# Kernel tuning notes

Measured on AMD Instinct MI355X. Metric: run time of the kernel, lower is better.

## Reference

```python
import jax, jax.numpy as jnp
import numpy as np


def setup_inputs() -> dict:
    key = jax.random.key(0)
    kq, kk, kv, km = jax.random.split(key, 4)
    B, H, N, D = 2, 16, 2048, 64
    q = jax.random.normal(kq, (B, H, N, D), dtype=jnp.float32)
    k = jax.random.normal(kk, (B, H, N, D), dtype=jnp.float32)
    v = jax.random.normal(kv, (B, H, N, D), dtype=jnp.float32)
    # mask > 0 means position is masked OUT (matches torch masked_fill(mask > 0, -max))
    mask = jax.random.randint(km, (B, N), 0, 2, dtype=jnp.int32)
    return {"q": q, "k": k, "v": v, "mask": mask}


def reference(q, k, v, mask):
    # q,k,v: [b,h,n,d]; mask: [b,j] with >0 = masked
    scale = q.shape[-1] ** -0.5
    sim = jnp.einsum('bhid,bhjd->bhij', q, k) * scale
    # l2_dist score modification: 2*qk*scale - ||q||^2 - ||k||^2
    q_sq = jnp.sum(q * q, axis=-1, keepdims=True)          # [b,h,i,1]
    k_sq = jnp.sum(k * k, axis=-1, keepdims=True)          # [b,h,j,1]
    sim = sim * 2 - q_sq - jnp.swapaxes(k_sq, -1, -2)       # [b,h,i,j]
    neg_max = -jnp.finfo(sim.dtype).max
    m = (mask > 0)[:, None, None, :]                        # [b,1,1,j]
    sim = jnp.where(m, neg_max, sim)
    attn = jax.nn.softmax(sim, axis=-1)
    out = jnp.einsum('bhij,bhjd->bhid', attn, v)
    return out
```

## Files before the change

kernel.cpp:

```cpp
#include <hip/hip_runtime.h>
#include <hip/hip_bf16.h>

#define NSEQ 2048
#define DD   64
#define HH   16
#define QT   128
#define KVB  64
#define NKV  (NSEQ / KVB)

typedef __attribute__((ext_vector_type(4)))  float f4;
typedef __attribute__((ext_vector_type(16))) float f32x16;
typedef __attribute__((ext_vector_type(8)))  short bf16x8;
typedef __attribute__((ext_vector_type(4)))  unsigned int u32x4;
typedef __attribute__((ext_vector_type(2)))  unsigned int u32x2;

#define QSCL  0.36067376022224085f
#define LOG2E 1.4426950408889634f
#define NEGBIG (-1.0e30f)
#define THR   8.0f

#define SWZ(row, q)  (((row) << 6) + ((((q) ^ ((row) & 7))) << 3))
#define SWZV(d, q)   (((d) << 6) + ((((q) ^ (((d) >> 2) & 7) ^ ((d) & 3))) << 3))

#if defined(__has_builtin)
#if __has_builtin(__builtin_amdgcn_exp2f)
#define EXP2F __builtin_amdgcn_exp2f
#endif
#if __has_builtin(__builtin_amdgcn_permlane32_swap)
#define HAVE_PLSWAP 1
#endif
#endif
#ifndef EXP2F
#define EXP2F exp2f
#endif

union bfu { u32x4 u; bf16x8 h; };

__device__ __forceinline__ unsigned cvtpk(float lo, float hi) {
    unsigned r;
    asm("v_cvt_pk_bf16_f32 %0, %1, %2" : "=v"(r) : "v"(lo), "v"(hi));
    return r;
}
template<int CTRL>
__device__ __forceinline__ float dppf(float x) {
    return __int_as_float(__builtin_amdgcn_update_dpp(
        0, __float_as_int(x), CTRL, 0xF, 0xF, true));
}
__device__ __forceinline__ float cross_max(float x) {
#ifdef HAVE_PLSWAP
    u32x2 r = __builtin_amdgcn_permlane32_swap(__float_as_uint(x), __float_as_uint(x),
                                               false, false);
    return fmaxf(__uint_as_float(r[0]), __uint_as_float(r[1]));
#else
    return fmaxf(x, __shfl_xor(x, 32));
#endif
}
__device__ __forceinline__ float cross_add(float x) {
#ifdef HAVE_PLSWAP
    u32x2 r = __builtin_amdgcn_permlane32_swap(__float_as_uint(x), __float_as_uint(x),
                                               false, false);
    return __uint_as_float(r[0]) + __uint_as_float(r[1]);
#else
    return x + __shfl_xor(x, 32);
#endif
}
__device__ __forceinline__ void pairmix(unsigned A, unsigned B,
                                        unsigned& d0, unsigned& d2, bool hi) {
#ifdef HAVE_PLSWAP
    u32x2 r = __builtin_amdgcn_permlane32_swap(A, B, false, false);
    d0 = r[0]; d2 = r[1];
#else
    unsigned v = hi ? A : B;
    unsigned x = (unsigned)__shfl_xor((int)v, 32);
    d0 = hi ? x : A;
    d2 = hi ? B : x;
#endif
}

__global__ __launch_bounds__(256, 2)
void attend_kernel(const float* __restrict__ qg, const float* __restrict__ kg,
                   const float* __restrict__ vg, const int* __restrict__ maskg,
                   float* __restrict__ outg)
{
    __shared__ __align__(16) unsigned short Ks[2][KVB * DD];
    __shared__ __align__(16) unsigned short Vt[2][KVB * DD];
    __shared__ __align__(16) float bias_s[2][KVB];

    const int t    = threadIdx.x;
    const int w    = t >> 6;
    const int lane = t & 63;
    const int c5   = lane & 31;
    const int g2   = lane >> 5;

    const int p     = blockIdx.x;
    const int bh    = (p & 7) * 4 + ((p >> 3) >> 4);
    const int qtile = (p >> 3) & 15;
    const int b     = bh >> 4;

    const size_t base = (size_t)bh * NSEQ * DD;
    const float* kp = kg + base;
    const float* vp = vg + base;
    const int*   mp = maskg + b * NSEQ;

    bfu qf[4];
    {
        const float* qp = qg + base + (size_t)(qtile*QT + w*32 + c5) * DD;
        #pragma unroll
        for (int ck = 0; ck < 4; ++ck) {
            f4 a  = *(const f4*)(qp + ck*16 + g2*8);
            f4 bb = *(const f4*)(qp + ck*16 + g2*8 + 4);
            qf[ck].u = (u32x4){ cvtpk(a[0]*QSCL,  a[1]*QSCL),  cvtpk(a[2]*QSCL,  a[3]*QSCL),
                                cvtpk(bb[0]*QSCL, bb[1]*QSCL), cvtpk(bb[2]*QSCL, bb[3]*QSCL) };
        }
    }

    f32x16 acc0, acc1;
    #pragma unroll
    for (int r = 0; r < 16; ++r) { acc0[r] = 0.f; acc1[r] = 0.f; }
    float m_run = NEGBIG, l_run = 0.f;

    const bool isK = (w < 2);
    const int  jK  = t >> 1;
    const int  kq0 = (t & 1) * 4;
    const int  uv  = t & 127;
    const int  dq  = uv & 15;
    const int  jq  = uv >> 4;

    f4  st[8];
    int mr = 0;

    auto loadTile = [&](int gt) {
        const int j0 = gt * KVB;
        if (isK) {
            const float* src = kp + (size_t)(j0 + jK) * DD + kq0 * 8;
            #pragma unroll
            for (int i2 = 0; i2 < 8; ++i2) st[i2] = ((const f4*)src)[i2];
            mr = mp[j0 + jK];
        } else {
            #pragma unroll
            for (int i2 = 0; i2 < 8; ++i2)
                st[i2] = *(const f4*)(vp + (size_t)(j0 + jq*8 + i2) * DD + dq*4);
        }
    };

    auto stageTile = [&](int bsel) {
        if (isK) {
            float sq = 0.f;
            #pragma unroll
            for (int i2 = 0; i2 < 8; ++i2)
                sq += st[i2][0]*st[i2][0] + st[i2][1]*st[i2][1]
                    + st[i2][2]*st[i2][2] + st[i2][3]*st[i2][3];
            sq += dppf<0xB1>(sq);
            if ((t & 1) == 0) bias_s[bsel][jK] = (mr > 0) ? NEGBIG : -sq * LOG2E;
            #pragma unroll
            for (int s2 = 0; s2 < 4; ++s2) {
                u32x4 kk = (u32x4){ cvtpk(st[2*s2][0],   st[2*s2][1]),
                                    cvtpk(st[2*s2][2],   st[2*s2][3]),
                                    cvtpk(st[2*s2+1][0], st[2*s2+1][1]),
                                    cvtpk(st[2*s2+1][2], st[2*s2+1][3]) };
                *(u32x4*)&Ks[bsel][SWZ(jK, kq0 + s2)] = kk;
            }
        } else {
            #pragma unroll
            for (int cc = 0; cc < 4; ++cc) {
                int d = dq*4 + cc;
                u32x4 tv = (u32x4){ cvtpk(st[0][cc], st[1][cc]),
                                    cvtpk(st[2][cc], st[3][cc]),
                                    cvtpk(st[4][cc], st[5][cc]),
                                    cvtpk(st[6][cc], st[7][cc]) };
                *(u32x4*)&Vt[bsel][SWZV(d, jq)] = tv;
            }
        }
    };

    loadTile(0);
    stageTile(0);
    loadTile(1);
    __syncthreads();

    int cur = 0;
    for (int kt = 0; kt < NKV; ++kt) {
        if (kt + 1 < NKV) stageTile(cur ^ 1);
        if (kt + 2 < NKV) loadTile(kt + 2);

        f32x16 s01[2];
        #pragma unroll
        for (int jt = 0; jt < 2; ++jt) {
            f4 b4[4];
            #pragma unroll
            for (int q = 0; q < 4; ++q)
                b4[q] = *(const f4*)&bias_s[cur][32*jt + 8*q + 4*g2];
            f32x16 sc;
            #pragma unroll
            for (int r = 0; r < 16; ++r) sc[r] = b4[r>>2][r&3];
            __builtin_amdgcn_s_setprio(1);
            #pragma unroll
            for (int ck = 0; ck < 4; ++ck) {
                bfu kb;
                kb.u = *(const u32x4*)&Ks[cur][SWZ(32*jt + c5, 2*ck + g2)];
                sc = __builtin_amdgcn_mfma_f32_32x32x16_bf16(kb.h, qf[ck].h, sc, 0, 0, 0);
            }
            __builtin_amdgcn_s_setprio(0);
            s01[jt] = sc;
        }

        float pmax;
        {
            float mm[8];
            #pragma unroll
            for (int i2 = 0; i2 < 8; ++i2)
                mm[i2] = fmaxf(fmaxf(s01[0][2*i2], s01[0][2*i2+1]),
                               fmaxf(s01[1][2*i2], s01[1][2*i2+1]));
            float ma = fmaxf(fmaxf(mm[0], mm[1]), fmaxf(mm[2], mm[3]));
            float mb = fmaxf(fmaxf(mm[4], mm[5]), fmaxf(mm[6], mm[7]));
            pmax = fmaxf(ma, mb);
        }
        pmax = cross_max(pmax);
        if (!__all(pmax <= m_run + THR)) {
            float mn = fmaxf(m_run, pmax);
            float corr = EXP2F(m_run - mn);
            m_run = mn;
            l_run *= corr;
            #pragma unroll
            for (int r = 0; r < 16; ++r) { acc0[r] *= corr; acc1[r] *= corr; }
        }

        unsigned Wp[16];
        float ls0 = 0.f, ls1 = 0.f;
        #pragma unroll
        for (int jt = 0; jt < 2; ++jt) {
            #pragma unroll
            for (int m = 0; m < 8; ++m) {
                float e0 = EXP2F(s01[jt][2*m]   - m_run);
                float e1 = EXP2F(s01[jt][2*m+1] - m_run);
                if (m & 1) ls1 += e0 + e1; else ls0 += e0 + e1;
                Wp[jt*8 + m] = cvtpk(e0, e1);
            }
        }
        l_run += cross_add(ls0 + ls1);

        const bool hi = (g2 != 0);
        __builtin_amdgcn_s_setprio(1);
        #pragma unroll
        for (int ck = 0; ck < 4; ++ck) {
            const int bs = (ck >> 1) * 8 + 4 * (ck & 1);
            unsigned d00, d20, d01, d21;
            pairmix(Wp[bs],   Wp[bs+2], d00, d20, hi);
            pairmix(Wp[bs+1], Wp[bs+3], d01, d21, hi);
            bfu pb;
            pb.u = (u32x4){ d00, d01, d20, d21 };
            bfu va0, va1;
            va0.u = *(const u32x4*)&Vt[cur][SWZV(     c5, 2*ck + g2)];
            va1.u = *(const u32x4*)&Vt[cur][SWZV(32 + c5, 2*ck + g2)];
            acc0 = __builtin_amdgcn_mfma_f32_32x32x16_bf16(va0.h, pb.h, acc0, 0, 0, 0);
            acc1 = __builtin_amdgcn_mfma_f32_32x32x16_bf16(va1.h, pb.h, acc1, 0, 0, 0);
        }
        __builtin_amdgcn_s_setprio(0);

        __syncthreads();
        cur ^= 1;
    }

    float inv = 1.0f / l_run;
    float* op = outg + base + (size_t)(qtile*QT + w*32 + c5) * DD;
    #pragma unroll
    for (int dt = 0; dt < 2; ++dt) {
        const f32x16 A = dt ? acc1 : acc0;
        #pragma unroll
        for (int q = 0; q < 4; ++q) {
            f4 o = { A[4*q]*inv, A[4*q+1]*inv, A[4*q+2]*inv, A[4*q+3]*inv };
            *(f4*)(op + 32*dt + 8*q + 4*g2) = o;
        }
    }
}

extern "C" void kernel_launch(void* const* d_in, const int* in_sizes, int n_in,
                              void* d_out, int out_size, void* d_ws, size_t ws_size,
                              hipStream_t stream) {
    const float* q    = (const float*)d_in[0];
    const float* k    = (const float*)d_in[1];
    const float* v    = (const float*)d_in[2];
    const int*   mask = (const int*)d_in[3];
    float* out = (float*)d_out;
    attend_kernel<<<dim3(512), dim3(256), 0, stream>>>(q, k, v, mask, out);
}
```

Before: 63.80 us.

## Process two KV tiles per iteration with doubled shared buffers and split staging

Each loop iteration now processes two 64-key tiles (128 keys): both QK^T products, one combined max and rescale check, softmax for both, then two PV passes. Shared K/V/bias buffers double in size so a pair of tiles can be staged per phase, with staging of the next pair split into two halves interleaved around the softmax. This halves the barriers and running-max rescale checks per key, and overlaps global loads with more compute. The cost is more shared memory and more registers, which may threaten the two-blocks-per-CU occupancy.

```diff
diff --git a/kernel.cpp b/kernel.cpp
--- a/kernel.cpp
+++ b/kernel.cpp
@@ -7,6 +7,7 @@
 #define QT   128
 #define KVB  64
 #define NKV  (NSEQ / KVB)
+#define NR   (NKV / 2)
 
 typedef __attribute__((ext_vector_type(4)))  float f4;
 typedef __attribute__((ext_vector_type(16))) float f32x16;
@@ -82,9 +83,9 @@
                    const float* __restrict__ vg, const int* __restrict__ maskg,
                    float* __restrict__ outg)
 {
-    __shared__ __align__(16) unsigned short Ks[2][KVB * DD];
-    __shared__ __align__(16) unsigned short Vt[2][KVB * DD];
-    __shared__ __align__(16) float bias_s[2][KVB];
+    __shared__ __align__(16) unsigned short Ks[2][2 * KVB * DD];
+    __shared__ __align__(16) unsigned short Vt[2][2 * KVB * DD];
+    __shared__ __align__(16) float bias_s[2][2 * KVB];
 
     const int t    = threadIdx.x;
     const int w    = t >> 6;
@@ -92,9 +93,9 @@
     const int c5   = lane & 31;
     const int g2   = lane >> 5;
 
-    const int p     = blockIdx.x;
-    const int bh    = (p & 7) * 4 + ((p >> 3) >> 4);
-    const int qtile = (p >> 3) & 15;
+    const int p0    = blockIdx.x;
+    const int bh    = (p0 & 7) * 4 + ((p0 >> 3) >> 4);
+    const int qtile = (p0 >> 3) & 15;
     const int b     = bh >> 4;
 
     const size_t base = (size_t)bh * NSEQ * DD;
@@ -143,7 +144,7 @@
         }
     };
 
-    auto stageTile = [&](int bsel) {
+    auto stageTile = [&](int pbuf, int tsub) {
         if (isK) {
             float sq = 0.f;
             #pragma unroll
@@ -151,14 +152,14 @@
                 sq += st[i2][0]*st[i2][0] + st[i2][1]*st[i2][1]
                     + st[i2][2]*st[i2][2] + st[i2][3]*st[i2][3];
             sq += dppf<0xB1>(sq);
-            if ((t & 1) == 0) bias_s[bsel][jK] = (mr > 0) ? NEGBIG : -sq * LOG2E;
+            if ((t & 1) == 0) bias_s[pbuf][tsub*KVB + jK] = (mr > 0) ? NEGBIG : -sq * LOG2E;
             #pragma unroll
             for (int s2 = 0; s2 < 4; ++s2) {
                 u32x4 kk = (u32x4){ cvtpk(st[2*s2][0],   st[2*s2][1]),
                                     cvtpk(st[2*s2][2],   st[2*s2][3]),
                                     cvtpk(st[2*s2+1][0], st[2*s2+1][1]),
                                     cvtpk(st[2*s2+1][2], st[2*s2+1][3]) };
-                *(u32x4*)&Ks[bsel][SWZ(jK, kq0 + s2)] = kk;
+                *(u32x4*)&Ks[pbuf][tsub*(KVB*DD) + SWZ(jK, kq0 + s2)] = kk;
             }
         } else {
             #pragma unroll
@@ -168,49 +169,57 @@
                                     cvtpk(st[2][cc], st[3][cc]),
                                     cvtpk(st[4][cc], st[5][cc]),
                                     cvtpk(st[6][cc], st[7][cc]) };
-                *(u32x4*)&Vt[bsel][SWZV(d, jq)] = tv;
+                *(u32x4*)&Vt[pbuf][tsub*(KVB*DD) + SWZV(d, jq)] = tv;
             }
         }
     };
 
-    loadTile(0);
-    stageTile(0);
-    loadTile(1);
+    loadTile(0); stageTile(0, 0);
+    loadTile(1); stageTile(0, 1);
+    loadTile(2);
     __syncthreads();
 
-    int cur = 0;
-    for (int kt = 0; kt < NKV; ++kt) {
-        if (kt + 1 < NKV) stageTile(cur ^ 1);
-        if (kt + 2 < NKV) loadTile(kt + 2);
-
-        f32x16 s01[2];
-        #pragma unroll
-        for (int jt = 0; jt < 2; ++jt) {
-            f4 b4[4];
-            #pragma unroll
-            for (int q = 0; q < 4; ++q)
-                b4[q] = *(const f4*)&bias_s[cur][32*jt + 8*q + 4*g2];
-            f32x16 sc;
-            #pragma unroll
-            for (int r = 0; r < 16; ++r) sc[r] = b4[r>>2][r&3];
-            __builtin_amdgcn_s_setprio(1);
-            #pragma unroll
-            for (int ck = 0; ck < 4; ++ck) {
-                bfu kb;
-                kb.u = *(const u32x4*)&Ks[cur][SWZ(32*jt + c5, 2*ck + g2)];
-                sc = __builtin_amdgcn_mfma_f32_32x32x16_bf16(kb.h, qf[ck].h, sc, 0, 0, 0);
-            }
-            __builtin_amdgcn_s_setprio(0);
-            s01[jt] = sc;
-        }
+    for (int r = 0; r < NR; ++r) {
+        const int p = r & 1;
+
+        if (r + 1 < NR) { stageTile(p ^ 1, 0); loadTile(2*r + 3); }
+
+        auto qkt = [&](int tsub, f32x16* sOut) {
+            #pragma unroll
+            for (int jt = 0; jt < 2; ++jt) {
+                f4 b4[4];
+                #pragma unroll
+                for (int q = 0; q < 4; ++q)
+                    b4[q] = *(const f4*)&bias_s[p][tsub*KVB + 32*jt + 8*q + 4*g2];
+                f32x16 sc;
+                #pragma unroll
+                for (int rr = 0; rr < 16; ++rr) sc[rr] = b4[rr>>2][rr&3];
+                __builtin_amdgcn_s_setprio(1);
+                #pragma unroll
+                for (int ck = 0; ck < 4; ++ck) {
+                    bfu kb;
+                    kb.u = *(const u32x4*)&Ks[p][tsub*(KVB*DD) + SWZ(32*jt + c5, 2*ck + g2)];
+                    sc = __builtin_amdgcn_mfma_f32_32x32x16_bf16(kb.h, qf[ck].h, sc, 0, 0, 0);
+                }
+                __builtin_amdgcn_s_setprio(0);
+                sOut[jt] = sc;
+            }
+        };
+        f32x16 sA[2], sB[2];
+        qkt(0, sA);
+        qkt(1, sB);
 
         float pmax;
         {
             float mm[8];
             #pragma unroll
-            for (int i2 = 0; i2 < 8; ++i2)
-                mm[i2] = fmaxf(fmaxf(s01[0][2*i2], s01[0][2*i2+1]),
-                               fmaxf(s01[1][2*i2], s01[1][2*i2+1]));
+            for (int i2 = 0; i2 < 8; ++i2) {
+                float a0 = fmaxf(fmaxf(sA[0][2*i2], sA[0][2*i2+1]),
+                                 fmaxf(sA[1][2*i2], sA[1][2*i2+1]));
+                float b0 = fmaxf(fmaxf(sB[0][2*i2], sB[0][2*i2+1]),
+                                 fmaxf(sB[1][2*i2], sB[1][2*i2+1]));
+                mm[i2] = fmaxf(a0, b0);
+            }
             float ma = fmaxf(fmaxf(mm[0], mm[1]), fmaxf(mm[2], mm[3]));
             float mb = fmaxf(fmaxf(mm[4], mm[5]), fmaxf(mm[6], mm[7]));
             pmax = fmaxf(ma, mb);
@@ -222,43 +231,62 @@
             m_run = mn;
             l_run *= corr;
             #pragma unroll
-            for (int r = 0; r < 16; ++r) { acc0[r] *= corr; acc1[r] *= corr; }
-        }
-
-        unsigned Wp[16];
-        float ls0 = 0.f, ls1 = 0.f;
-        #pragma unroll
-        for (int jt = 0; jt < 2; ++jt) {
-            #pragma unroll
-            for (int m = 0; m < 8; ++m) {
-                float e0 = EXP2F(s01[jt][2*m]   - m_run);
-                float e1 = EXP2F(s01[jt][2*m+1] - m_run);
-                if (m & 1) ls1 += e0 + e1; else ls0 += e0 + e1;
-                Wp[jt*8 + m] = cvtpk(e0, e1);
-            }
-        }
-        l_run += cross_add(ls0 + ls1);
+            for (int rr = 0; rr < 16; ++rr) { acc0[rr] *= corr; acc1[rr] *= corr; }
+        }
+
+        unsigned WpA[16], WpB[16];
+        float ls = 0.f;
+        {
+            float l0 = 0.f, l1 = 0.f;
+            #pragma unroll
+            for (int jt = 0; jt < 2; ++jt) {
+                #pragma unroll
+                for (int m = 0; m < 8; ++m) {
+                    float e0 = EXP2F(sA[jt][2*m]   - m_run);
+                    float e1 = EXP2F(sA[jt][2*m+1] - m_run);
+                    if (m & 1) l1 += e0 + e1; else l0 += e0 + e1;
+                    WpA[jt*8 + m] = cvtpk(e0, e1);
+                }
+            }
+            #pragma unroll
+            for (int jt = 0; jt < 2; ++jt) {
+                #pragma unroll
+                for (int m = 0; m < 8; ++m) {
+                    float e0 = EXP2F(sB[jt][2*m]   - m_run);
+                    float e1 = EXP2F(sB[jt][2*m+1] - m_run);
+                    if (m & 1) l1 += e0 + e1; else l0 += e0 + e1;
+                    WpB[jt*8 + m] = cvtpk(e0, e1);
+                }
+            }
+            ls = l0 + l1;
+        }
+        l_run += cross_add(ls);
+
+        if (r + 1 < NR) { stageTile(p ^ 1, 1); if (r + 2 < NR) loadTile(2*r + 4); }
 
         const bool hi = (g2 != 0);
-        __builtin_amdgcn_s_setprio(1);
-        #pragma unroll
-        for (int ck = 0; ck < 4; ++ck) {
-            const int bs = (ck >> 1) * 8 + 4 * (ck & 1);
-            unsigned d00, d20, d01, d21;
-            pairmix(Wp[bs],   Wp[bs+2], d00, d20, hi);
-            pairmix(Wp[bs+1], Wp[bs+3], d01, d21, hi);
-            bfu pb;
-            pb.u = (u32x4){ d00, d01, d20, d21 };
-            bfu va0, va1;
-            va0.u = *(const u32x4*)&Vt[cur][SWZV(     c5, 2*ck + g2)];
-            va1.u = *(const u32x4*)&Vt[cur][SWZV(32 + c5, 2*ck + g2)];
-            acc0 = __builtin_amdgcn_mfma_f32_32x32x16_bf16(va0.h, pb.h, acc0, 0, 0, 0);
-            acc1 = __builtin_amdgcn_mfma_f32_32x32x16_bf16(va1.h, pb.h, acc1, 0, 0, 0);
-        }
-        __builtin_amdgcn_s_setprio(0);
+        auto pv = [&](int tsub, unsigned* Wp) {
+            __builtin_amdgcn_s_setprio(1);
+            #pragma unroll
+            for (int ck = 0; ck < 4; ++ck) {
+                const int bs = (ck >> 1) * 8 + 4 * (ck & 1);
+                unsigned d00, d20, d01, d21;
+                pairmix(Wp[bs],   Wp[bs+2], d00, d20, hi);
+                pairmix(Wp[bs+1], Wp[bs+3], d01, d21, hi);
+                bfu pb;
+                pb.u = (u32x4){ d00, d01, d20, d21 };
+                bfu va0, va1;
+                va0.u = *(const u32x4*)&Vt[p][tsub*(KVB*DD) + SWZV(     c5, 2*ck + g2)];
+                va1.u = *(const u32x4*)&Vt[p][tsub*(KVB*DD) + SWZV(32 + c5, 2*ck + g2)];
+                acc0 = __builtin_amdgcn_mfma_f32_32x32x16_bf16(va0.h, pb.h, acc0, 0, 0, 0);
+                acc1 = __builtin_amdgcn_mfma_f32_32x32x16_bf16(va1.h, pb.h, acc1, 0, 0, 0);
+            }
+            __builtin_amdgcn_s_setprio(0);
+        };
+        pv(0, WpA);
+        pv(1, WpB);
 
         __syncthreads();
-        cur ^= 1;
     }
 
     float inv = 1.0f / l_run;
```

Result: no change. 63.46 us (-0.5%).

## Split block into producer and consumer warps for K/V staging

Applied to the files above, without the earlier changes.

Doubles the block to 512 threads: four waves now only compute attention, and four dedicated producer waves load K/V from global memory, convert them to bf16 and stage them into the double-buffered LDS tiles one step ahead. The consumer waves no longer hold staging registers or issue global loads, so their register pressure drops and their MFMA work can overlap with the producers' fetching. In exchange the producers' loads are no longer prefetched two tiles ahead, launch bounds change to 512x4 (which may cap registers), and the extra waves use occupancy slots.

```diff
diff --git a/kernel.cpp b/kernel.cpp
--- a/kernel.cpp
+++ b/kernel.cpp
@@ -77,7 +77,7 @@
 #endif
 }
 
-__global__ __launch_bounds__(256, 2)
+__global__ __launch_bounds__(512, 4)
 void attend_kernel(const float* __restrict__ qg, const float* __restrict__ kg,
                    const float* __restrict__ vg, const int* __restrict__ maskg,
                    float* __restrict__ outg)
@@ -91,6 +91,7 @@
     const int lane = t & 63;
     const int c5   = lane & 31;
     const int g2   = lane >> 5;
+    const bool isProd = (w >= 4);
 
     const int p     = blockIdx.x;
     const int bh    = (p & 7) * 4 + ((p >> 3) >> 4);
@@ -103,7 +104,9 @@
     const int*   mp = maskg + b * NSEQ;
 
     bfu qf[4];
-    {
+    f32x16 acc0, acc1;
+    float m_run = NEGBIG, l_run = 0.f;
+    if (!isProd) {
         const float* qp = qg + base + (size_t)(qtile*QT + w*32 + c5) * DD;
         #pragma unroll
         for (int ck = 0; ck < 4; ++ck) {
@@ -112,46 +115,32 @@
             qf[ck].u = (u32x4){ cvtpk(a[0]*QSCL,  a[1]*QSCL),  cvtpk(a[2]*QSCL,  a[3]*QSCL),
                                 cvtpk(bb[0]*QSCL, bb[1]*QSCL), cvtpk(bb[2]*QSCL, bb[3]*QSCL) };
         }
+        #pragma unroll
+        for (int r = 0; r < 16; ++r) { acc0[r] = 0.f; acc1[r] = 0.f; }
     }
 
-    f32x16 acc0, acc1;
-    #pragma unroll
-    for (int r = 0; r < 16; ++r) { acc0[r] = 0.f; acc1[r] = 0.f; }
-    float m_run = NEGBIG, l_run = 0.f;
-
-    const bool isK = (w < 2);
-    const int  jK  = t >> 1;
-    const int  kq0 = (t & 1) * 4;
-    const int  uv  = t & 127;
+    const int  u   = t & 255;
+    const bool isK = (u < 128);
+    const int  jK  = u >> 1;
+    const int  kq0 = (u & 1) * 4;
+    const int  uv  = u & 127;
     const int  dq  = uv & 15;
     const int  jq  = uv >> 4;
 
-    f4  st[8];
-    int mr = 0;
-
-    auto loadTile = [&](int gt) {
-        const int j0 = gt * KVB;
+    auto prodTile = [&](int gt, int bsel) {
+        f4 st[8];
         if (isK) {
-            const float* src = kp + (size_t)(j0 + jK) * DD + kq0 * 8;
+            const float* src = kp + (size_t)(gt*KVB + jK) * DD + kq0 * 8;
             #pragma unroll
             for (int i2 = 0; i2 < 8; ++i2) st[i2] = ((const f4*)src)[i2];
-            mr = mp[j0 + jK];
-        } else {
-            #pragma unroll
-            for (int i2 = 0; i2 < 8; ++i2)
-                st[i2] = *(const f4*)(vp + (size_t)(j0 + jq*8 + i2) * DD + dq*4);
-        }
-    };
-
-    auto stageTile = [&](int bsel) {
-        if (isK) {
+            int mr = mp[gt*KVB + jK];
             float sq = 0.f;
             #pragma unroll
             for (int i2 = 0; i2 < 8; ++i2)
                 sq += st[i2][0]*st[i2][0] + st[i2][1]*st[i2][1]
                     + st[i2][2]*st[i2][2] + st[i2][3]*st[i2][3];
             sq += dppf<0xB1>(sq);
-            if ((t & 1) == 0) bias_s[bsel][jK] = (mr > 0) ? NEGBIG : -sq * LOG2E;
+            if ((u & 1) == 0) bias_s[bsel][jK] = (mr > 0) ? NEGBIG : -sq * LOG2E;
             #pragma unroll
             for (int s2 = 0; s2 < 4; ++s2) {
                 u32x4 kk = (u32x4){ cvtpk(st[2*s2][0],   st[2*s2][1]),
@@ -161,6 +150,9 @@
                 *(u32x4*)&Ks[bsel][SWZ(jK, kq0 + s2)] = kk;
             }
         } else {
+            #pragma unroll
+            for (int i2 = 0; i2 < 8; ++i2)
+                st[i2] = *(const f4*)(vp + (size_t)(gt*KVB + jq*8 + i2) * DD + dq*4);
             #pragma unroll
             for (int cc = 0; cc < 4; ++cc) {
                 int d = dq*4 + cc;
@@ -173,103 +165,104 @@
         }
     };
 
-    loadTile(0);
-    stageTile(0);
-    loadTile(1);
+    if (isProd) prodTile(0, 0);
     __syncthreads();
 
-    int cur = 0;
     for (int kt = 0; kt < NKV; ++kt) {
-        if (kt + 1 < NKV) stageTile(cur ^ 1);
-        if (kt + 2 < NKV) loadTile(kt + 2);
-
-        f32x16 s01[2];
+        const int kc = kt & 1;
+
+        if (isProd) {
+            if (kt + 1 < NKV) prodTile(kt + 1, kc ^ 1);
+        } else {
+            f32x16 s01[2];
+            #pragma unroll
+            for (int jt = 0; jt < 2; ++jt) {
+                f4 b4[4];
+                #pragma unroll
+                for (int q = 0; q < 4; ++q)
+                    b4[q] = *(const f4*)&bias_s[kc][32*jt + 8*q + 4*g2];
+                f32x16 sc;
+                #pragma unroll
+                for (int r = 0; r < 16; ++r) sc[r] = b4[r>>2][r&3];
+                __builtin_amdgcn_s_setprio(1);
+                #pragma unroll
+                for (int ck = 0; ck < 4; ++ck) {
+                    bfu kb;
+                    kb.u = *(const u32x4*)&Ks[kc][SWZ(32*jt + c5, 2*ck + g2)];
+                    sc = __builtin_amdgcn_mfma_f32_32x32x16_bf16(kb.h, qf[ck].h, sc, 0, 0, 0);
+                }
+                __builtin_amdgcn_s_setprio(0);
+                s01[jt] = sc;
+            }
+
+            float pmax;
+            {
+                float mm[8];
+                #pragma unroll
+                for (int i2 = 0; i2 < 8; ++i2)
+                    mm[i2] = fmaxf(fmaxf(s01[0][2*i2], s01[0][2*i2+1]),
+                                   fmaxf(s01[1][2*i2], s01[1][2*i2+1]));
+                float ma = fmaxf(fmaxf(mm[0], mm[1]), fmaxf(mm[2], mm[3]));
+                float mb = fmaxf(fmaxf(mm[4], mm[5]), fmaxf(mm[6], mm[7]));
+                pmax = fmaxf(ma, mb);
+            }
+            pmax = cross_max(pmax);
+            if (!__all(pmax <= m_run + THR)) {
+                float mn = fmaxf(m_run, pmax);
+                float corr = EXP2F(m_run - mn);
+                m_run = mn;
+                l_run *= corr;
+                #pragma unroll
+                for (int r = 0; r < 16; ++r) { acc0[r] *= corr; acc1[r] *= corr; }
+            }
+
+            unsigned Wp[16];
+            float ls0 = 0.f, ls1 = 0.f;
+            #pragma unroll
+            for (int jt = 0; jt < 2; ++jt) {
+                #pragma unroll
+                for (int m = 0; m < 8; ++m) {
+                    float e0 = EXP2F(s01[jt][2*m]   - m_run);
+                    float e1 = EXP2F(s01[jt][2*m+1] - m_run);
+                    if (m & 1) ls1 += e0 + e1; else ls0 += e0 + e1;
+                    Wp[jt*8 + m] = cvtpk(e0, e1);
+                }
+            }
+            l_run += cross_add(ls0 + ls1);
+
+            const bool hi = (g2 != 0);
+            __builtin_amdgcn_s_setprio(1);
+            #pragma unroll
+            for (int ck = 0; ck < 4; ++ck) {
+                const int bs = (ck >> 1) * 8 + 4 * (ck & 1);
+                unsigned d00, d20, d01, d21;
+                pairmix(Wp[bs],   Wp[bs+2], d00, d20, hi);
+                pairmix(Wp[bs+1], Wp[bs+3], d01, d21, hi);
+                bfu pb;
+                pb.u = (u32x4){ d00, d01, d20, d21 };
+                bfu va0, va1;
+                va0.u = *(const u32x4*)&Vt[kc][SWZV(     c5, 2*ck + g2)];
+                va1.u = *(const u32x4*)&Vt[kc][SWZV(32 + c5, 2*ck + g2)];
+                acc0 = __builtin_amdgcn_mfma_f32_32x32x16_bf16(va0.h, pb.h, acc0, 0, 0, 0);
+                acc1 = __builtin_amdgcn_mfma_f32_32x32x16_bf16(va1.h, pb.h, acc1, 0, 0, 0);
+            }
+            __builtin_amdgcn_s_setprio(0);
+        }
+
+        __syncthreads();
+    }
+
+    if (!isProd) {
+        float inv = 1.0f / l_run;
+        float* op = outg + base + (size_t)(qtile*QT + w*32 + c5) * DD;
         #pragma unroll
-        for (int jt = 0; jt < 2; ++jt) {
-            f4 b4[4];
-            #pragma unroll
-            for (int q = 0; q < 4; ++q)
-                b4[q] = *(const f4*)&bias_s[cur][32*jt + 8*q + 4*g2];
-            f32x16 sc;
-            #pragma unroll
-            for (int r = 0; r < 16; ++r) sc[r] = b4[r>>2][r&3];
-            __builtin_amdgcn_s_setprio(1);
-            #pragma unroll
-            for (int ck = 0; ck < 4; ++ck) {
-                bfu kb;
-                kb.u = *(const u32x4*)&Ks[cur][SWZ(32*jt + c5, 2*ck + g2)];
-                sc = __builtin_amdgcn_mfma_f32_32x32x16_bf16(kb.h, qf[ck].h, sc, 0, 0, 0);
-            }
-            __builtin_amdgcn_s_setprio(0);
-            s01[jt] = sc;
-        }
-
-        float pmax;
-        {
-            float mm[8];
-            #pragma unroll
-            for (int i2 = 0; i2 < 8; ++i2)
-                mm[i2] = fmaxf(fmaxf(s01[0][2*i2], s01[0][2*i2+1]),
-                               fmaxf(s01[1][2*i2], s01[1][2*i2+1]));
-            float ma = fmaxf(fmaxf(mm[0], mm[1]), fmaxf(mm[2], mm[3]));
-            float mb = fmaxf(fmaxf(mm[4], mm[5]), fmaxf(mm[6], mm[7]));
-            pmax = fmaxf(ma, mb);
-        }
-        pmax = cross_max(pmax);
-        if (!__all(pmax <= m_run + THR)) {
-            float mn = fmaxf(m_run, pmax);
-            float corr = EXP2F(m_run - mn);
-            m_run = mn;
-            l_run *= corr;
-            #pragma unroll
-            for (int r = 0; r < 16; ++r) { acc0[r] *= corr; acc1[r] *= corr; }
-        }
-
-        unsigned Wp[16];
-        float ls0 = 0.f, ls1 = 0.f;
-        #pragma unroll
-        for (int jt = 0; jt < 2; ++jt) {
-            #pragma unroll
-            for (int m = 0; m < 8; ++m) {
-                float e0 = EXP2F(s01[jt][2*m]   - m_run);
-                float e1 = EXP2F(s01[jt][2*m+1] - m_run);
-                if (m & 1) ls1 += e0 + e1; else ls0 += e0 + e1;
-                Wp[jt*8 + m] = cvtpk(e0, e1);
-            }
-        }
-        l_run += cross_add(ls0 + ls1);
-
-        const bool hi = (g2 != 0);
-        __builtin_amdgcn_s_setprio(1);
-        #pragma unroll
-        for (int ck = 0; ck < 4; ++ck) {
-            const int bs = (ck >> 1) * 8 + 4 * (ck & 1);
-            unsigned d00, d20, d01, d21;
-            pairmix(Wp[bs],   Wp[bs+2], d00, d20, hi);
-            pairmix(Wp[bs+1], Wp[bs+3], d01, d21, hi);
-            bfu pb;
-            pb.u = (u32x4){ d00, d01, d20, d21 };
-            bfu va0, va1;
-            va0.u = *(const u32x4*)&Vt[cur][SWZV(     c5, 2*ck + g2)];
-            va1.u = *(const u32x4*)&Vt[cur][SWZV(32 + c5, 2*ck + g2)];
-            acc0 = __builtin_amdgcn_mfma_f32_32x32x16_bf16(va0.h, pb.h, acc0, 0, 0, 0);
-            acc1 = __builtin_amdgcn_mfma_f32_32x32x16_bf16(va1.h, pb.h, acc1, 0, 0, 0);
-        }
-        __builtin_amdgcn_s_setprio(0);
-
-        __syncthreads();
-        cur ^= 1;
-    }
-
-    float inv = 1.0f / l_run;
-    float* op = outg + base + (size_t)(qtile*QT + w*32 + c5) * DD;
-    #pragma unroll
-    for (int dt = 0; dt < 2; ++dt) {
-        const f32x16 A = dt ? acc1 : acc0;
-        #pragma unroll
-        for (int q = 0; q < 4; ++q) {
-            f4 o = { A[4*q]*inv, A[4*q+1]*inv, A[4*q+2]*inv, A[4*q+3]*inv };
-            *(f4*)(op + 32*dt + 8*q + 4*g2) = o;
+        for (int dt = 0; dt < 2; ++dt) {
+            const f32x16 A = dt ? acc1 : acc0;
+            #pragma unroll
+            for (int q = 0; q < 4; ++q) {
+                f4 o = { A[4*q]*inv, A[4*q+1]*inv, A[4*q+2]*inv, A[4*q+3]*inv };
+                *(f4*)(op + 32*dt + 8*q + 4*g2) = o;
+            }
         }
     }
 }
@@ -282,5 +275,5 @@
     const float* v    = (const float*)d_in[2];
     const int*   mask = (const int*)d_in[3];
     float* out = (float*)d_out;
-    attend_kernel<<<dim3(512), dim3(256), 0, stream>>>(q, k, v, mask, out);
-}
+    attend_kernel<<<dim3(512), dim3(512), 0, stream>>>(q, k, v, mask, out);
+}
```

After: 64.75 us. No clear change (+1.5%).

## Pre-convert K/V to bf16 fragment images in workspace and drop LDS staging

Applied to the files above, without the earlier changes.

Adds a prep kernel that converts K and V to bf16 once per call. It writes them in workspace laid out in the exact MFMA fragment order, together with a precomputed mask/norm bias. The main kernel then reads its fragments straight from global memory into registers, prefetching the next K tile, and no longer needs shared memory or per-tile __syncthreads. This removes the fp32 K/V traffic and conversion work that was repeated across 16 q-tiles. The cost is an extra launch and workspace traffic, and it relies on L2 for reuse. A fallback to the original kernel runs if the workspace is too small.

```diff
diff --git a/kernel.cpp b/kernel.cpp
--- a/kernel.cpp
+++ b/kernel.cpp
@@ -7,6 +7,9 @@
 #define QT   128
 #define KVB  64
 #define NKV  (NSEQ / KVB)
+#define NBH  32
+#define TILE_SH 4096
+#define KIMG_BYTES ((size_t)NBH * NKV * TILE_SH * 2)
 
 typedef __attribute__((ext_vector_type(4)))  float f4;
 typedef __attribute__((ext_vector_type(16))) float f32x16;
@@ -77,15 +80,74 @@
 #endif
 }
 
-__global__ __launch_bounds__(256, 2)
-void attend_kernel(const float* __restrict__ qg, const float* __restrict__ kg,
-                   const float* __restrict__ vg, const int* __restrict__ maskg,
-                   float* __restrict__ outg)
+__global__ __launch_bounds__(256)
+void prep_kernel(const float* __restrict__ kg, const float* __restrict__ vg,
+                 const int* __restrict__ maskg,
+                 unsigned short* __restrict__ Kimg,
+                 unsigned short* __restrict__ Vimg,
+                 float* __restrict__ biasg)
 {
-    __shared__ __align__(16) unsigned short Ks[2][KVB * DD];
-    __shared__ __align__(16) unsigned short Vt[2][KVB * DD];
-    __shared__ __align__(16) float bias_s[2][KVB];
-
+    int blk = blockIdx.x;
+    const bool doV = (blk >= NBH * NKV);
+    if (doV) blk -= NBH * NKV;
+    const int bh   = blk >> 5;
+    const int tile = blk & 31;
+    const int tid  = threadIdx.x;
+
+    if (!doV) {
+        __shared__ float bsum[64];
+        const float* kp = kg + ((size_t)bh * NSEQ + tile * KVB) * DD;
+        unsigned short* out = Kimg + (size_t)blk * TILE_SH;
+        if (tid < 64) bsum[tid] = 0.f;
+        __syncthreads();
+        #pragma unroll
+        for (int cc = 0; cc < 2; ++cc) {
+            int c  = tid + cc * 256;
+            int c5 = c & 31, g2 = (c >> 5) & 1, ck = (c >> 6) & 3, jt = c >> 8;
+            const float* src = kp + (size_t)(32*jt + c5) * DD + 16*ck + 8*g2;
+            f4 a = ((const f4*)src)[0];
+            f4 b = ((const f4*)src)[1];
+            u32x4 kk = (u32x4){ cvtpk(a[0],a[1]), cvtpk(a[2],a[3]),
+                                cvtpk(b[0],b[1]), cvtpk(b[2],b[3]) };
+            *(u32x4*)&out[c * 8] = kk;
+            float sq = a[0]*a[0]+a[1]*a[1]+a[2]*a[2]+a[3]*a[3]
+                     + b[0]*b[0]+b[1]*b[1]+b[2]*b[2]+b[3]*b[3];
+            atomicAdd(&bsum[32*jt + c5], sq);
+        }
+        __syncthreads();
+        if (tid < 64) {
+            int j  = tile * KVB + tid;
+            int b_ = bh >> 4;
+            biasg[bh * NSEQ + j] =
+                (maskg[b_ * NSEQ + j] > 0) ? NEGBIG : -bsum[tid] * LOG2E;
+        }
+    } else {
+        const float* vp = vg + ((size_t)bh * NSEQ + tile * KVB) * DD;
+        unsigned short* out = Vimg + (size_t)blk * TILE_SH;
+        #pragma unroll
+        for (int cc = 0; cc < 2; ++cc) {
+            int c  = tid + cc * 256;
+            int c5 = c & 31, dt = (c >> 5) & 1, g2 = (c >> 6) & 1, ck = c >> 7;
+            int d  = dt * 32 + c5;
+            int j0 = 16*ck + 8*g2;
+            float v0 = vp[(size_t)(j0+0)*DD + d], v1 = vp[(size_t)(j0+1)*DD + d];
+            float v2 = vp[(size_t)(j0+2)*DD + d], v3 = vp[(size_t)(j0+3)*DD + d];
+            float v4 = vp[(size_t)(j0+4)*DD + d], v5 = vp[(size_t)(j0+5)*DD + d];
+            float v6 = vp[(size_t)(j0+6)*DD + d], v7 = vp[(size_t)(j0+7)*DD + d];
+            u32x4 tv = (u32x4){ cvtpk(v0,v1), cvtpk(v2,v3),
+                                cvtpk(v4,v5), cvtpk(v6,v7) };
+            *(u32x4*)&out[c * 8] = tv;
+        }
+    }
+}
+
+__global__ __launch_bounds__(256)
+void attend_main(const unsigned short* __restrict__ Kimg,
+                 const unsigned short* __restrict__ Vimg,
+                 const float* __restrict__ biasg,
+                 const float* __restrict__ qg,
+                 float* __restrict__ outg)
+{
     const int t    = threadIdx.x;
     const int w    = t >> 6;
     const int lane = t & 63;
@@ -95,12 +157,11 @@
     const int p     = blockIdx.x;
     const int bh    = (p & 7) * 4 + ((p >> 3) >> 4);
     const int qtile = (p >> 3) & 15;
-    const int b     = bh >> 4;
 
     const size_t base = (size_t)bh * NSEQ * DD;
-    const float* kp = kg + base;
-    const float* vp = vg + base;
-    const int*   mp = maskg + b * NSEQ;
+    const unsigned short* kimg = Kimg + (size_t)bh * NKV * TILE_SH;
+    const unsigned short* vimg = Vimg + (size_t)bh * NKV * TILE_SH;
+    const float* bias_bh = biasg + bh * NSEQ;
 
     bfu qf[4];
     {
@@ -114,6 +175,161 @@
         }
     }
 
+    f32x16 acc0, acc1;
+    #pragma unroll
+    for (int r = 0; r < 16; ++r) { acc0[r] = 0.f; acc1[r] = 0.f; }
+    float m_run = NEGBIG, l_run = 0.f;
+
+    u32x4 kbA[8], kbB[8];
+    #pragma unroll
+    for (int jt = 0; jt < 2; ++jt)
+        #pragma unroll
+        for (int ck = 0; ck < 4; ++ck)
+            kbA[jt*4+ck] = *(const u32x4*)&kimg[(size_t)((((jt*4+ck)*2+g2)*32 + c5) * 8)];
+
+    auto round = [&](int kt, u32x4 (&kbC)[8], u32x4 (&kbN)[8]) {
+        f32x16 s01[2];
+        #pragma unroll
+        for (int jt = 0; jt < 2; ++jt) {
+            f4 b4[4];
+            #pragma unroll
+            for (int q = 0; q < 4; ++q)
+                b4[q] = *(const f4*)&bias_bh[kt*KVB + 32*jt + 8*q + 4*g2];
+            f32x16 sc;
+            #pragma unroll
+            for (int r = 0; r < 16; ++r) sc[r] = b4[r>>2][r&3];
+            __builtin_amdgcn_s_setprio(1);
+            #pragma unroll
+            for (int ck = 0; ck < 4; ++ck) {
+                bfu kb; kb.u = kbC[jt*4+ck];
+                sc = __builtin_amdgcn_mfma_f32_32x32x16_bf16(kb.h, qf[ck].h, sc, 0, 0, 0);
+            }
+            __builtin_amdgcn_s_setprio(0);
+            s01[jt] = sc;
+        }
+
+        const unsigned short* vt = vimg + (size_t)kt * TILE_SH;
+        u32x4 vau[8];
+        #pragma unroll
+        for (int ck = 0; ck < 4; ++ck)
+            #pragma unroll
+            for (int dt = 0; dt < 2; ++dt)
+                vau[ck*2+dt] = *(const u32x4*)&vt[(size_t)(((((ck*2+g2)*2)+dt)*32 + c5) * 8)];
+
+        if (kt + 1 < NKV) {
+            const unsigned short* kn = kimg + (size_t)(kt+1) * TILE_SH;
+            #pragma unroll
+            for (int jt = 0; jt < 2; ++jt)
+                #pragma unroll
+                for (int ck = 0; ck < 4; ++ck)
+                    kbN[jt*4+ck] = *(const u32x4*)&kn[(size_t)((((jt*4+ck)*2+g2)*32 + c5) * 8)];
+        }
+
+        float pmax;
+        {
+            float mm[8];
+            #pragma unroll
+            for (int i2 = 0; i2 < 8; ++i2)
+                mm[i2] = fmaxf(fmaxf(s01[0][2*i2], s01[0][2*i2+1]),
+                               fmaxf(s01[1][2*i2], s01[1][2*i2+1]));
+            float ma = fmaxf(fmaxf(mm[0], mm[1]), fmaxf(mm[2], mm[3]));
+            float mb = fmaxf(fmaxf(mm[4], mm[5]), fmaxf(mm[6], mm[7]));
+            pmax = fmaxf(ma, mb);
+        }
+        pmax = cross_max(pmax);
+        if (!__all(pmax <= m_run + THR)) {
+            float mn = fmaxf(m_run, pmax);
+            float corr = EXP2F(m_run - mn);
+            m_run = mn;
+            l_run *= corr;
+            #pragma unroll
+            for (int r = 0; r < 16; ++r) { acc0[r] *= corr; acc1[r] *= corr; }
+        }
+
+        unsigned Wp[16];
+        float ls0 = 0.f, ls1 = 0.f;
+        #pragma unroll
+        for (int jt = 0; jt < 2; ++jt) {
+            #pragma unroll
+            for (int m = 0; m < 8; ++m) {
+                float e0 = EXP2F(s01[jt][2*m]   - m_run);
+                float e1 = EXP2F(s01[jt][2*m+1] - m_run);
+                if (m & 1) ls1 += e0 + e1; else ls0 += e0 + e1;
+                Wp[jt*8 + m] = cvtpk(e0, e1);
+            }
+        }
+        l_run += cross_add(ls0 + ls1);
+
+        const bool hi = (g2 != 0);
+        __builtin_amdgcn_s_setprio(1);
+        #pragma unroll
+        for (int ck = 0; ck < 4; ++ck) {
+            const int bs = (ck >> 1) * 8 + 4 * (ck & 1);
+            unsigned d00, d20, d01, d21;
+            pairmix(Wp[bs],   Wp[bs+2], d00, d20, hi);
+            pairmix(Wp[bs+1], Wp[bs+3], d01, d21, hi);
+            bfu pb; pb.u = (u32x4){ d00, d01, d20, d21 };
+            bfu va0, va1;
+            va0.u = vau[ck*2+0];
+            va1.u = vau[ck*2+1];
+            acc0 = __builtin_amdgcn_mfma_f32_32x32x16_bf16(va0.h, pb.h, acc0, 0, 0, 0);
+            acc1 = __builtin_amdgcn_mfma_f32_32x32x16_bf16(va1.h, pb.h, acc1, 0, 0, 0);
+        }
+        __builtin_amdgcn_s_setprio(0);
+    };
+
+    for (int k2 = 0; k2 < NKV; k2 += 2) {
+        round(k2,     kbA, kbB);
+        round(k2 + 1, kbB, kbA);
+    }
+
+    float inv = 1.0f / l_run;
+    float* op = outg + base + (size_t)(qtile*QT + w*32 + c5) * DD;
+    #pragma unroll
+    for (int dt = 0; dt < 2; ++dt) {
+        const f32x16 A = dt ? acc1 : acc0;
+        #pragma unroll
+        for (int q = 0; q < 4; ++q) {
+            f4 o = { A[4*q]*inv, A[4*q+1]*inv, A[4*q+2]*inv, A[4*q+3]*inv };
+            *(f4*)(op + 32*dt + 8*q + 4*g2) = o;
+        }
+    }
+}
+
+__global__ __launch_bounds__(256, 2)
+void attend_fallback(const float* __restrict__ qg, const float* __restrict__ kg,
+                     const float* __restrict__ vg, const int* __restrict__ maskg,
+                     float* __restrict__ outg)
+{
+    __shared__ __align__(16) unsigned short Ks[2][KVB * DD];
+    __shared__ __align__(16) unsigned short Vt[2][KVB * DD];
+    __shared__ __align__(16) float bias_s[2][KVB];
+
+    const int t    = threadIdx.x;
+    const int w    = t >> 6;
+    const int lane = t & 63;
+    const int c5   = lane & 31;
+    const int g2   = lane >> 5;
+    const int p     = blockIdx.x;
+    const int bh    = (p & 7) * 4 + ((p >> 3) >> 4);
+    const int qtile = (p >> 3) & 15;
+    const int b     = bh >> 4;
+    const size_t base = (size_t)bh * NSEQ * DD;
+    const float* kp = kg + base;
+    const float* vp = vg + base;
+    const int*   mp = maskg + b * NSEQ;
+
+    bfu qf[4];
+    {
+        const float* qp = qg + base + (size_t)(qtile*QT + w*32 + c5) * DD;
+        #pragma unroll
+        for (int ck = 0; ck < 4; ++ck) {
+            f4 a  = *(const f4*)(qp + ck*16 + g2*8);
+            f4 bb = *(const f4*)(qp + ck*16 + g2*8 + 4);
+            qf[ck].u = (u32x4){ cvtpk(a[0]*QSCL,  a[1]*QSCL),  cvtpk(a[2]*QSCL,  a[3]*QSCL),
+                                cvtpk(bb[0]*QSCL, bb[1]*QSCL), cvtpk(bb[2]*QSCL, bb[3]*QSCL) };
+        }
+    }
     f32x16 acc0, acc1;
     #pragma unroll
     for (int r = 0; r < 16; ++r) { acc0[r] = 0.f; acc1[r] = 0.f; }
@@ -125,7 +341,6 @@
     const int  uv  = t & 127;
     const int  dq  = uv & 15;
     const int  jq  = uv >> 4;
-
     f4  st[8];
     int mr = 0;
 
@@ -142,7 +357,6 @@
                 st[i2] = *(const f4*)(vp + (size_t)(j0 + jq*8 + i2) * DD + dq*4);
         }
     };
-
     auto stageTile = [&](int bsel) {
         if (isK) {
             float sq = 0.f;
@@ -173,16 +387,12 @@
         }
     };
 
-    loadTile(0);
-    stageTile(0);
-    loadTile(1);
+    loadTile(0); stageTile(0); loadTile(1);
     __syncthreads();
-
     int cur = 0;
     for (int kt = 0; kt < NKV; ++kt) {
         if (kt + 1 < NKV) stageTile(cur ^ 1);
         if (kt + 2 < NKV) loadTile(kt + 2);
-
         f32x16 s01[2];
         #pragma unroll
         for (int jt = 0; jt < 2; ++jt) {
@@ -203,7 +413,6 @@
             __builtin_amdgcn_s_setprio(0);
             s01[jt] = sc;
         }
-
         float pmax;
         {
             float mm[8];
@@ -219,12 +428,10 @@
         if (!__all(pmax <= m_run + THR)) {
             float mn = fmaxf(m_run, pmax);
             float corr = EXP2F(m_run - mn);
-            m_run = mn;
-            l_run *= corr;
+            m_run = mn; l_run *= corr;
             #pragma unroll
             for (int r = 0; r < 16; ++r) { acc0[r] *= corr; acc1[r] *= corr; }
         }
-
         unsigned Wp[16];
         float ls0 = 0.f, ls1 = 0.f;
         #pragma unroll
@@ -238,7 +445,6 @@
             }
         }
         l_run += cross_add(ls0 + ls1);
-
         const bool hi = (g2 != 0);
         __builtin_amdgcn_s_setprio(1);
         #pragma unroll
@@ -247,8 +453,7 @@
             unsigned d00, d20, d01, d21;
             pairmix(Wp[bs],   Wp[bs+2], d00, d20, hi);
             pairmix(Wp[bs+1], Wp[bs+3], d01, d21, hi);
-            bfu pb;
-            pb.u = (u32x4){ d00, d01, d20, d21 };
+            bfu pb; pb.u = (u32x4){ d00, d01, d20, d21 };
             bfu va0, va1;
             va0.u = *(const u32x4*)&Vt[cur][SWZV(     c5, 2*ck + g2)];
             va1.u = *(const u32x4*)&Vt[cur][SWZV(32 + c5, 2*ck + g2)];
@@ -256,11 +461,9 @@
             acc1 = __builtin_amdgcn_mfma_f32_32x32x16_bf16(va1.h, pb.h, acc1, 0, 0, 0);
         }
         __builtin_amdgcn_s_setprio(0);
-
         __syncthreads();
         cur ^= 1;
     }
-
     float inv = 1.0f / l_run;
     float* op = outg + base + (size_t)(qtile*QT + w*32 + c5) * DD;
     #pragma unroll
@@ -282,5 +485,18 @@
     const float* v    = (const float*)d_in[2];
     const int*   mask = (const int*)d_in[3];
     float* out = (float*)d_out;
-    attend_kernel<<<dim3(512), dim3(256), 0, stream>>>(q, k, v, mask, out);
-}
+
+    const size_t biasBytes = (size_t)NBH * NSEQ * sizeof(float);
+    const size_t needed    = 2 * KIMG_BYTES + biasBytes;
+    if (ws_size >= needed) {
+        unsigned short* Kimg = (unsigned short*)d_ws;
+        unsigned short* Vimg = (unsigned short*)((char*)d_ws + KIMG_BYTES);
+        float* biasg = (float*)((char*)d_ws + 2 * KIMG_BYTES);
+        prep_kernel<<<dim3(2 * NBH * NKV), dim3(256), 0, stream>>>(
+            k, v, mask, Kimg, Vimg, biasg);
+        attend_main<<<dim3(512), dim3(256), 0, stream>>>(
+            Kimg, Vimg, biasg, q, out);
+    } else {
+        attend_fallback<<<dim3(512), dim3(256), 0, stream>>>(q, k, v, mask, out);
+    }
+}
```

Result: slower. 76.93 us (+20.6%).
